# Kernel tuning notes

Hardware: AMD Instinct MI355X
Metric: run time of the kernel (lower is better)

Reference implementation:

```python
import jax, jax.numpy as jnp
import numpy as np
from jax import lax


def run_gru(seq, w_ih, w_hh, b_ih, b_hh):
    """PyTorch-convention GRU. seq: (T, N, E) -> outputs (T, N, H), h0 = 0."""
    H = w_hh.shape[1]
    gx = jnp.einsum('tne,ge->tng', seq, w_ih) + b_ih  # (T, N, 3H), precomputed input gates

    def step(h, gx_t):
        gh = h @ w_hh.T + b_hh
        xr, xz, xn = jnp.split(gx_t, 3, axis=-1)
        hr, hz, hn = jnp.split(gh, 3, axis=-1)
        r = jax.nn.sigmoid(xr + hr)
        z = jax.nn.sigmoid(xz + hz)
        n = jnp.tanh(xn + r * hn)
        h_new = (1.0 - z) * n + z * h
        return h_new, h_new

    h0 = jnp.zeros((seq.shape[1], H), dtype=seq.dtype)
    _, hs = lax.scan(step, h0, gx)
    return hs


def setup_inputs() -> dict:
    key = jax.random.key(0)
    ks = jax.random.split(key, 20)
    B, T, I, E, Ha, Hb, O = 32, 64, 256, 256, 256, 256, 1
    s = 0.05
    return {
        'x': jax.random.normal(ks[0], (B, T, I), dtype=jnp.float32),
        'emb_w': jax.random.normal(ks[1], (E, I), dtype=jnp.float32) * s,
        'emb_b': jax.random.normal(ks[2], (E,), dtype=jnp.float32) * s,
        'a_wih': jax.random.normal(ks[3], (3 * Ha, E), dtype=jnp.float32) * s,
        'a_whh': jax.random.normal(ks[4], (3 * Ha, Ha), dtype=jnp.float32) * s,
        'a_bih': jax.random.normal(ks[5], (3 * Ha,), dtype=jnp.float32) * s,
        'a_bhh': jax.random.normal(ks[6], (3 * Ha,), dtype=jnp.float32) * s,
        'b_wih': jax.random.normal(ks[7], (3 * Hb, E), dtype=jnp.float32) * s,
        'b_whh': jax.random.normal(ks[8], (3 * Hb, Hb), dtype=jnp.float32) * s,
        'b_bih': jax.random.normal(ks[9], (3 * Hb,), dtype=jnp.float32) * s,
        'b_bhh': jax.random.normal(ks[10], (3 * Hb,), dtype=jnp.float32) * s,
        'alpha_w': jax.random.normal(ks[11], (1, Ha), dtype=jnp.float32) * s,
        'alpha_b': jax.random.normal(ks[12], (1,), dtype=jnp.float32) * s,
        'beta_w': jax.random.normal(ks[13], (E, Hb), dtype=jnp.float32) * s,
        'beta_b': jax.random.normal(ks[14], (E,), dtype=jnp.float32) * s,
        'out_w': jax.random.normal(ks[15], (O, E), dtype=jnp.float32) * s,
        'out_b': jax.random.normal(ks[16], (O,), dtype=jnp.float32) * s,
    }


def reference(x, emb_w, emb_b, a_wih, a_whh, a_bih, a_bhh,
              b_wih, b_whh, b_bih, b_bhh, alpha_w, alpha_b,
              beta_w, beta_b, out_w, out_b):
    B, T, I = x.shape
    P = T - 1  # prefix lengths 1..T-1
    xt = jnp.transpose(x, (1, 0, 2))               # (T, B, I) time-major
    emb = jnp.einsum('tbi,ei->tbe', xt, emb_w) + emb_b  # (T, B, E)
    E = emb.shape[-1]

    # Reversed prefix p (length t=p+1): rev[p, k] = emb[p - k] for k < t, else 0.
    idx = jnp.arange(P)[:, None] - jnp.arange(T)[None, :]   # (P, T)
    valid = idx >= 0
    idxc = jnp.clip(idx, 0)
    rev = jnp.where(valid[:, :, None, None], emb[idxc], 0.0)  # (P, T, B, E)

    seq = jnp.transpose(rev, (1, 0, 2, 3)).reshape(T, P * B, E)  # (T, P*B, E)
    ha = run_gru(seq, a_wih, a_whh, a_bih, a_bhh)  # (T, P*B, Ha)
    hb = run_gru(seq, b_wih, b_whh, b_bih, b_bhh)  # (T, P*B, Hb)
    ha = jnp.transpose(ha.reshape(T, P, B, -1), (1, 0, 2, 3))  # (P, T, B, Ha)
    hb = jnp.transpose(hb.reshape(T, P, B, -1), (1, 0, 2, 3))

    # flip back within each prefix (same index map), then * 0.5 as in the source
    rows = jnp.arange(P)[:, None]
    fa = ha[rows, idxc] * 0.5   # (P, T, B, Ha); positions >= t are junk, masked below
    fb = hb[rows, idxc] * 0.5

    pre = jnp.einsum('ptbh,h->ptb', fa, alpha_w[0]) + alpha_b[0]
    logits = jnp.where(valid[:, :, None], pre, -jnp.inf)
    alpha = jax.nn.softmax(logits, axis=1)                       # softmax over time per prefix
    beta = jnp.tanh(jnp.einsum('ptbh,eh->ptbe', fb, beta_w) + beta_b)  # (P, T, B, E)

    # context: c_t = sum_j alpha * beta * emb[:t]  (alpha is 0 outside prefix)
    c = jnp.einsum('ptb,ptbe,tbe->pbe', alpha, beta, emb)        # (P, B, E)
    pred = (c @ out_w.T + out_b)                                  # (P, B, 1)
    pred = jnp.transpose(pred, (1, 0, 2))                         # (B, P, 1)

    # contribution weights; w_emb / w_out enter via .data in torch (no grad)
    w_emb = lax.stop_gradient(emb_w)
    w_out0 = lax.stop_gradient(out_w)[0]
    e = jnp.einsum('ptbe,e,ei->ptbi', beta, w_out0, w_emb)        # (P, T, B, I)
    denom = jnp.arange(1, P + 1, dtype=x.dtype)[:, None, None]    # mean over t visits
    g = jnp.einsum('ptb,ptbi,tbi->pbi', alpha, e, xt) / denom     # (P, B, I)
    weight = jnp.transpose(g, (1, 0, 2))                          # (B, P, I)
    return pred, weight
```

## Files before the change

kernel.cpp:

```cpp
#include <hip/hip_runtime.h>
#include <math.h>

#define B_   32
#define T_   64
#define P_   63
#define E_   256

typedef _Float16 half8 __attribute__((ext_vector_type(8)));
typedef _Float16 half4 __attribute__((ext_vector_type(4)));
typedef float    f32x4 __attribute__((ext_vector_type(4)));

__device__ __forceinline__ float sigmoidf_(float x) { return 1.0f / (1.0f + __expf(-x)); }
__device__ __forceinline__ float tanhfast_(float x) { float e = __expf(2.0f*x); return 1.0f - 2.0f/(e + 1.0f); }

__device__ __forceinline__ void barrier_lds_() {
    asm volatile("" ::: "memory");
    asm volatile("s_waitcnt lgkmcnt(0)" ::: "memory");
    __builtin_amdgcn_s_barrier();
    asm volatile("" ::: "memory");
}

__global__ __launch_bounds__(64) void k_prep(
    const float* __restrict__ awhh, const float* __restrict__ bwhh,
    const float* __restrict__ awih, const float* __restrict__ bwih,
    const float* __restrict__ beta_w, const float* __restrict__ emb_w, const float* __restrict__ out_w,
    _Float16* __restrict__ wfa, _Float16* __restrict__ wfb,
    _Float16* __restrict__ wifa, _Float16* __restrict__ wifb,
    _Float16* __restrict__ bwf, _Float16* __restrict__ mf)
{
    int bid = blockIdx.x, l = threadIdx.x;
    if (bid < 1664) {
        const float* W; _Float16* dst; float scale = 1.0f; int r;
        if (bid < 384)       { W = awhh;   dst = wfa;  r = bid; }
        else if (bid < 768)  { W = bwhh;   dst = wfb;  r = bid - 384; }
        else if (bid < 1152) { W = awih;   dst = wifa; r = bid - 768; }
        else if (bid < 1536) { W = bwih;   dst = wifb; r = bid - 1152; }
        else                 { W = beta_w; dst = bwf;  r = bid - 1536; scale = 0.5f; }
        int ot = r >> 3, kc = r & 7;
        int orow = ot * 16 + (l & 15);
        int c0   = kc * 32 + (l >> 4) * 8;
        half8 v;
        #pragma unroll
        for (int j = 0; j < 8; ++j) v[j] = (_Float16)(scale * W[(size_t)orow * 256 + c0 + j]);
        *reinterpret_cast<half8*>(&dst[((size_t)r * 64 + l) * 8]) = v;
    } else {
        int r = bid - 1664;
        int ot = r >> 3, kc = r & 7;
        int i  = ot * 16 + (l & 15);
        int e0 = kc * 32 + (l >> 4) * 8;
        half8 v;
        #pragma unroll
        for (int j = 0; j < 8; ++j) v[j] = (_Float16)(out_w[e0 + j] * emb_w[(size_t)(e0 + j) * 256 + i]);
        *reinterpret_cast<half8*>(&mf[((size_t)r * 64 + l) * 8]) = v;
    }
}

__global__ __launch_bounds__(256) void k_emb(const float* __restrict__ x,
                                             const float* __restrict__ emb_w,
                                             const float* __restrict__ emb_b,
                                             const float* __restrict__ out_w,
                                             _Float16* __restrict__ embh,
                                             _Float16* __restrict__ ewh,
                                             _Float16* __restrict__ xh) {
    int r0 = blockIdx.x * 8;
    int tid = threadIdx.x;
    __shared__ float xs[8][E_];
    for (int rr = 0; rr < 8; ++rr) {
        int row = r0 + rr, t = row >> 5, b = row & 31;
        float xv = x[((size_t)b * T_ + t) * E_ + tid];
        xs[rr][tid] = xv;
        xh[((size_t)b * T_ + t) * E_ + tid] = (_Float16)xv;
    }
    __syncthreads();
    float acc[8];
    #pragma unroll
    for (int rr = 0; rr < 8; ++rr) acc[rr] = 0.f;
    const float* wr = emb_w + (size_t)tid * E_;
    for (int c = 0; c < 256; c += 4) {
        float4 wv = *reinterpret_cast<const float4*>(wr + c);
        #pragma unroll
        for (int rr = 0; rr < 8; ++rr) {
            float4 ev = *reinterpret_cast<const float4*>(&xs[rr][c]);
            acc[rr] += wv.x * ev.x + wv.y * ev.y + wv.z * ev.z + wv.w * ev.w;
        }
    }
    float eb = emb_b[tid], ow = out_w[tid];
    #pragma unroll
    for (int rr = 0; rr < 8; ++rr) {
        float v = acc[rr] + eb;
        embh[(size_t)(r0 + rr) * E_ + tid] = (_Float16)v;
        ewh[(size_t)(r0 + rr) * E_ + tid]  = (_Float16)(v * ow);
    }
}

__global__ __launch_bounds__(512, 2) void k_gates2(
    const _Float16* __restrict__ embh,
    const _Float16* __restrict__ wifa, const _Float16* __restrict__ wifb,
    const float* __restrict__ abih, const float* __restrict__ abhh,
    const float* __restrict__ bbih, const float* __restrict__ bbhh,
    _Float16* __restrict__ gpa, _Float16* __restrict__ gpb)
{
    __shared__ _Float16 esw[32 * E_];
    int bid = blockIdx.x;
    int g = bid >> 6, t = bid & 63;
    const _Float16* wif = g ? wifb : wifa;
    const float* bih = g ? bbih : abih;
    const float* bhh = g ? bbhh : abhh;
    _Float16* gp = g ? gpb : gpa;
    int tid = threadIdx.x, w = tid >> 6, l = tid & 63, lg = l >> 4, lr = l & 15;

    #pragma unroll
    for (int q = 0; q < 2; ++q) {
        int idx = q * 512 + tid;
        int b = idx >> 5, e0 = (idx & 31) * 8;
        half8 v = *reinterpret_cast<const half8*>(&embh[((size_t)t * 32 + b) * E_ + e0]);
        *reinterpret_cast<half8*>(&esw[b * E_ + (e0 ^ ((b & 7) << 3))]) = v;
    }
    half8 aw[3][2][8];
    #pragma unroll
    for (int g3 = 0; g3 < 3; ++g3)
        #pragma unroll
        for (int i = 0; i < 2; ++i)
            #pragma unroll
            for (int kc = 0; kc < 8; ++kc)
                aw[g3][i][kc] = *reinterpret_cast<const half8*>(
                    &wif[(((size_t)(g3 * 16 + 2 * w + i) * 8 + kc) * 64 + l) * 8]);
    f32x4 acc[3][2][2];
    #pragma unroll
    for (int g3 = 0; g3 < 3; ++g3)
        #pragma unroll
        for (int i = 0; i < 2; ++i)
            #pragma unroll
            for (int rt = 0; rt < 2; ++rt)
                #pragma unroll
                for (int j = 0; j < 4; ++j) {
                    int d = g3 * 256 + 32 * w + 16 * i + lg * 4 + j;
                    acc[g3][i][rt][j] = bih[d] + ((g3 < 2) ? bhh[d] : 0.f);
                }
    __syncthreads();
    #pragma unroll
    for (int kc = 0; kc < 8; ++kc) {
        half8 eb[2];
        #pragma unroll
        for (int rt = 0; rt < 2; ++rt)
            eb[rt] = *reinterpret_cast<const half8*>(
                &esw[(rt * 16 + lr) * E_ + ((kc * 32 + lg * 8) ^ ((lr & 7) << 3))]);
        #pragma unroll
        for (int g3 = 0; g3 < 3; ++g3)
            #pragma unroll
            for (int i = 0; i < 2; ++i)
                #pragma unroll
                for (int rt = 0; rt < 2; ++rt)
                    acc[g3][i][rt] = __builtin_amdgcn_mfma_f32_16x16x32_f16(
                        aw[g3][i][kc], eb[rt], acc[g3][i][rt], 0, 0, 0);
    }
    #pragma unroll
    for (int g3 = 0; g3 < 3; ++g3)
        #pragma unroll
        for (int rt = 0; rt < 2; ++rt) {
            half8 v;
            #pragma unroll
            for (int i = 0; i < 2; ++i)
                #pragma unroll
                for (int j = 0; j < 4; ++j) v[i * 4 + j] = (_Float16)acc[g3][i][rt][j];
            *reinterpret_cast<half8*>(
                &gp[((((size_t)t * 2 + rt) * 8 + w) * 3 + g3) * 512 + l * 8]) = v;
        }
}

__global__ __launch_bounds__(512, 2) void k_gru_f(
    const _Float16* __restrict__ gpa, const _Float16* __restrict__ gpb,
    const _Float16* __restrict__ wfa, const _Float16* __restrict__ wfb,
    const float* __restrict__ abhh, const float* __restrict__ bbhh,
    const float* __restrict__ alpha_w, const float* __restrict__ alpha_b,
    float* __restrict__ pre, _Float16* __restrict__ hstore)
{
    extern __shared__ char smem[];
    half8*    wlds = reinterpret_cast<half8*>(smem);
    _Float16* hsp  = reinterpret_cast<_Float16*>(smem + 98304);
    float*    red  = reinterpret_cast<float*>(smem + 98304 + 16384);

    int bid = blockIdx.x;
    int p   = 62 - (bid >> 2);
    int g   = (bid >> 1) & 1;
    int bh  = bid & 1;
    int tid = threadIdx.x;
    int w = tid >> 6, l = tid & 63, lg = l >> 4, lr = l & 15;
    const _Float16* gp  = g ? gpb : gpa;
    const _Float16* wf  = g ? wfb : wfa;
    const float*    bhh = g ? bbhh : abhh;

    half8 wreg[3][2][6];
    #pragma unroll
    for (int g3 = 0; g3 < 3; ++g3)
        #pragma unroll
        for (int i = 0; i < 2; ++i) {
            int ot = g3 * 16 + 2 * w + i;
            #pragma unroll
            for (int kc = 0; kc < 6; ++kc)
                wreg[g3][i][kc] = *reinterpret_cast<const half8*>(&wf[((size_t)(ot * 8 + kc) * 64 + l) * 8]);
        }
    #pragma unroll
    for (int q = 0; q < 12; ++q) {
        int idx = q * 512 + tid;
        int ot = idx >> 7, kcs = (idx >> 6) & 1, l2 = idx & 63;
        wlds[idx] = *reinterpret_cast<const half8*>(&wf[((size_t)(ot * 8 + 6 + kcs) * 64 + l2) * 8]);
    }
    float bhn[2][4], awv[2][4];
    #pragma unroll
    for (int i = 0; i < 2; ++i)
        #pragma unroll
        for (int j = 0; j < 4; ++j) {
            int d = 32 * w + 16 * i + lg * 4 + j;
            bhn[i][j] = bhh[512 + d];
            awv[i][j] = alpha_w[d];
        }
    float ab = alpha_b[0];
    float hreg[2][4];
    #pragma unroll
    for (int i = 0; i < 2; ++i)
        #pragma unroll
        for (int j = 0; j < 4; ++j) hreg[i][j] = 0.f;
    __syncthreads();

    size_t tri = (size_t)p * (p + 1) / 2;

    for (int k = 0; k <= p; ++k) {
        int t_in = p - k;
        int wr = k & 1, rb = wr ^ 1;
        if (k > 0 && g == 0 && tid < 16) {
            float s = 0.f;
            #pragma unroll
            for (int q = 0; q < 8; ++q) s += red[(rb * 16 + tid) * 8 + q];
            pre[((size_t)p * T_ + (t_in + 1)) * B_ + bh * 16 + tid] = 0.5f * s + ab;
        }
        half8 gch[3];
        {
            const _Float16* gq = gp + (((size_t)(t_in * 2 + bh) * 8 + w) * 3) * 512 + l * 8;
            #pragma unroll
            for (int c = 0; c < 3; ++c)
                gch[c] = *reinterpret_cast<const half8*>(gq + (size_t)c * 512);
        }
        f32x4 acc[3][2];
        #pragma unroll
        for (int g3 = 0; g3 < 3; ++g3)
            #pragma unroll
            for (int i = 0; i < 2; ++i)
                #pragma unroll
                for (int j = 0; j < 4; ++j) acc[g3][i][j] = 0.f;
        if (k > 0) {
            half8 bhv[2];
            {
                int cb = (lg * 8) ^ ((lr & 7) << 3);
                bhv[0] = *reinterpret_cast<const half8*>(&hsp[(rb * 16 + lr) * 256 + cb]);
            }
            #pragma unroll
            for (int kc = 0; kc < 8; ++kc) {
                if (kc < 7) {
                    int cb = ((kc + 1) * 32 + lg * 8) ^ ((lr & 7) << 3);
                    bhv[(kc + 1) & 1] = *reinterpret_cast<const half8*>(&hsp[(rb * 16 + lr) * 256 + cb]);
                }
                if (kc < 6) {
                    #pragma unroll
                    for (int g3 = 0; g3 < 3; ++g3)
                        #pragma unroll
                        for (int i = 0; i < 2; ++i)
                            acc[g3][i] = __builtin_amdgcn_mfma_f32_16x16x32_f16(
                                wreg[g3][i][kc], bhv[kc & 1], acc[g3][i], 0, 0, 0);
                } else {
                    #pragma unroll
                    for (int g3 = 0; g3 < 3; ++g3)
                        #pragma unroll
                        for (int i = 0; i < 2; ++i) {
                            half8 wlv = wlds[((g3 * 16 + 2 * w + i) * 2 + (kc - 6)) * 64 + l];
                            acc[g3][i] = __builtin_amdgcn_mfma_f32_16x16x32_f16(
                                wlv, bhv[kc & 1], acc[g3][i], 0, 0, 0);
                        }
                }
            }
        }
        _Float16* hdst = hstore + ((tri + (size_t)k) * B_ + bh * 16 + lr) * (size_t)E_ + 32 * w + lg * 4;
        #pragma unroll
        for (int i = 0; i < 2; ++i) {
            half4 hh;
            #pragma unroll
            for (int j = 0; j < 4; ++j) {
                int e = i * 4 + j;
                float rg = sigmoidf_(acc[0][i][j] + (float)gch[0][e]);
                float zg = sigmoidf_(acc[1][i][j] + (float)gch[1][e]);
                float ng = tanhfast_((float)gch[2][e] + rg * (acc[2][i][j] + bhn[i][j]));
                float h  = (1.f - zg) * ng + zg * hreg[i][j];
                hreg[i][j] = h;
                hh[j] = (_Float16)h;
            }
            int ce = (32 * w + 16 * i + lg * 4) ^ ((lr & 7) << 3);
            *reinterpret_cast<half4*>(&hsp[(wr * 16 + lr) * 256 + ce]) = hh;
            if (g) *reinterpret_cast<half4*>(hdst + 16 * i) = hh;
        }
        if (!g) {
            float pa = 0.f;
            #pragma unroll
            for (int i = 0; i < 2; ++i)
                #pragma unroll
                for (int j = 0; j < 4; ++j) pa += hreg[i][j] * awv[i][j];
            pa += __shfl_xor(pa, 16, 64);
            pa += __shfl_xor(pa, 32, 64);
            if (l < 16) red[(wr * 16 + l) * 8 + w] = pa;
        }
        barrier_lds_();
    }
    if (g == 0 && tid < 16) {
        int wl = p & 1;
        float s = 0.f;
        #pragma unroll
        for (int q = 0; q < 8; ++q) s += red[(wl * 16 + tid) * 8 + q];
        pre[((size_t)p * T_ + 0) * B_ + bh * 16 + tid] = 0.5f * s + ab;
    }
}

__global__ __launch_bounds__(256, 1) void k_att(
    const _Float16* __restrict__ hH,
    const _Float16* __restrict__ bwf, const _Float16* __restrict__ mf,
    const float* __restrict__ beta_b,
    const float* __restrict__ pre,
    const _Float16* __restrict__ ewh, const _Float16* __restrict__ xh,
    const float* __restrict__ out_b,
    float* __restrict__ out)
{
    extern __shared__ char smem[];
    _Float16* hs   = reinterpret_cast<_Float16*>(smem);
    _Float16* es   = reinterpret_cast<_Float16*>(smem + 32768);
    _Float16* xs   = reinterpret_cast<_Float16*>(smem + 65536);
    float*    alds = reinterpret_cast<float*>(smem + 98304);
    float*    red  = reinterpret_cast<float*>(smem + 98304 + 256);
    int tid = threadIdx.x, w = tid >> 6, l = tid & 63, lg = l >> 4, lr = l & 15;

    half8 aw[4][8], am[4][8];
    #pragma unroll
    for (int ot = 0; ot < 4; ++ot)
        #pragma unroll
        for (int kc = 0; kc < 8; ++kc) {
            size_t fo = (((size_t)(4 * w + ot) * 8 + kc) * 64 + l) * 8;
            aw[ot][kc] = *reinterpret_cast<const half8*>(&bwf[fo]);
            am[ot][kc] = *reinterpret_cast<const half8*>(&mf[fo]);
        }
    float bb[4][4];
    #pragma unroll
    for (int ot = 0; ot < 4; ++ot)
        #pragma unroll
        for (int j = 0; j < 4; ++j)
            bb[ot][j] = beta_b[(4 * w + ot) * 16 + lg * 4 + j];
    float ob = out_b[0];

    for (int it = 0; it < 8; ++it) {
        int pair = blockIdx.x * 8 + it;
        int p = pair >> 5, b = pair & 31;
        size_t tri = (size_t)p * (p + 1) / 2;
        {
            int kr = tid >> 5, l32 = tid & 31, e0 = l32 * 8;
            #pragma unroll
            for (int q = 0; q < 8; ++q) {
                int k = q * 8 + kr;
                int sw = e0 ^ ((k & 7) << 3);
                half8 hv, ev;
                if (k <= p) {
                    hv = *reinterpret_cast<const half8*>(&hH[((tri + (size_t)(p - k)) * B_ + b) * 256 + e0]);
                    ev = *reinterpret_cast<const half8*>(&ewh[((size_t)k * B_ + b) * 256 + e0]);
                } else {
                    #pragma unroll
                    for (int j = 0; j < 8; ++j) { hv[j] = (_Float16)0.f; ev[j] = (_Float16)0.f; }
                }
                *reinterpret_cast<half8*>(&hs[k * 256 + sw]) = hv;
                *reinterpret_cast<half8*>(&es[k * 256 + sw]) = ev;
                *reinterpret_cast<half8*>(&xs[k * 256 + sw]) =
                    *reinterpret_cast<const half8*>(&xh[((size_t)b * T_ + k) * 256 + e0]);
            }
        }
        if (tid < 64) {
            float v = (tid <= p) ? pre[((size_t)p * T_ + tid) * B_ + b] : -3.4e38f;
            float m = v;
            #pragma unroll
            for (int off = 32; off > 0; off >>= 1) m = fmaxf(m, __shfl_xor(m, off, 64));
            float e = (tid <= p) ? __expf(v - m) : 0.f;
            float s = e;
            #pragma unroll
            for (int off = 32; off > 0; off >>= 1) s += __shfl_xor(s, off, 64);
            alds[tid] = e / s;
        }
        __syncthreads();
        f32x4 acc[4][4];
        #pragma unroll
        for (int ot = 0; ot < 4; ++ot)
            #pragma unroll
            for (int rt = 0; rt < 4; ++rt)
                #pragma unroll
                for (int j = 0; j < 4; ++j) acc[ot][rt][j] = bb[ot][j];
        #pragma unroll
        for (int kc = 0; kc < 8; ++kc) {
            half8 hb[4];
            #pragma unroll
            for (int rt = 0; rt < 4; ++rt)
                hb[rt] = *reinterpret_cast<const half8*>(&hs[(rt * 16 + lr) * 256 + ((kc * 32 + lg * 8) ^ ((lr & 7) << 3))]);
            #pragma unroll
            for (int ot = 0; ot < 4; ++ot)
                #pragma unroll
                for (int rt = 0; rt < 4; ++rt)
                    acc[ot][rt] = __builtin_amdgcn_mfma_f32_16x16x32_f16(aw[ot][kc], hb[rt], acc[ot][rt], 0, 0, 0);
        }
        float pv = 0.f;
        half4 ureg[4][4];
        #pragma unroll
        for (int ot = 0; ot < 4; ++ot)
            #pragma unroll
            for (int rt = 0; rt < 4; ++rt) {
                int k = rt * 16 + lr;
                float al = alds[k];
                int d0 = (4 * w + ot) * 16 + lg * 4;
                half4 ev4 = *reinterpret_cast<const half4*>(&es[k * 256 + (d0 ^ ((lr & 7) << 3))]);
                #pragma unroll
                for (int j = 0; j < 4; ++j) {
                    float u = al * tanhfast_(acc[ot][rt][j]);
                    ureg[ot][rt][j] = (_Float16)u;
                    pv += u * (float)ev4[j];
                }
            }
        __syncthreads();
        #pragma unroll
        for (int ot = 0; ot < 4; ++ot)
            #pragma unroll
            for (int rt = 0; rt < 4; ++rt) {
                int k = rt * 16 + lr;
                int d0 = (4 * w + ot) * 16 + lg * 4;
                *reinterpret_cast<half4*>(&hs[k * 256 + (d0 ^ ((lr & 7) << 3))]) = ureg[ot][rt];
            }
        #pragma unroll
        for (int off = 1; off < 64; off <<= 1) pv += __shfl_xor(pv, off, 64);
        if (l == 0) red[w] = pv;
        __syncthreads();
        if (tid == 0) out[(size_t)b * P_ + p] = red[0] + red[1] + red[2] + red[3] + ob;
        f32x4 a2[4][4];
        #pragma unroll
        for (int ot = 0; ot < 4; ++ot)
            #pragma unroll
            for (int rt = 0; rt < 4; ++rt)
                #pragma unroll
                for (int j = 0; j < 4; ++j) a2[ot][rt][j] = 0.f;
        #pragma unroll
        for (int kc = 0; kc < 8; ++kc) {
            half8 ub[4];
            #pragma unroll
            for (int rt = 0; rt < 4; ++rt)
                ub[rt] = *reinterpret_cast<const half8*>(&hs[(rt * 16 + lr) * 256 + ((kc * 32 + lg * 8) ^ ((lr & 7) << 3))]);
            #pragma unroll
            for (int ot = 0; ot < 4; ++ot)
                #pragma unroll
                for (int rt = 0; rt < 4; ++rt)
                    a2[ot][rt] = __builtin_amdgcn_mfma_f32_16x16x32_f16(am[ot][kc], ub[rt], a2[ot][rt], 0, 0, 0);
        }
        float r4[4][4];
        #pragma unroll
        for (int ot = 0; ot < 4; ++ot)
            #pragma unroll
            for (int j = 0; j < 4; ++j) r4[ot][j] = 0.f;
        #pragma unroll
        for (int ot = 0; ot < 4; ++ot)
            #pragma unroll
            for (int rt = 0; rt < 4; ++rt) {
                int k = rt * 16 + lr;
                int i0 = (4 * w + ot) * 16 + lg * 4;
                half4 xv4 = *reinterpret_cast<const half4*>(&xs[k * 256 + (i0 ^ ((lr & 7) << 3))]);
                #pragma unroll
                for (int j = 0; j < 4; ++j) r4[ot][j] += a2[ot][rt][j] * (float)xv4[j];
            }
        #pragma unroll
        for (int off = 1; off < 16; off <<= 1)
            #pragma unroll
            for (int ot = 0; ot < 4; ++ot)
                #pragma unroll
                for (int j = 0; j < 4; ++j) r4[ot][j] += __shfl_xor(r4[ot][j], off, 64);
        if (lr == 0) {
            float inv = 1.f / (float)(p + 1);
            #pragma unroll
            for (int ot = 0; ot < 4; ++ot) {
                f32x4 v;
                #pragma unroll
                for (int j = 0; j < 4; ++j) v[j] = r4[ot][j] * inv;
                *reinterpret_cast<f32x4*>(&out[2016 + ((size_t)b * P_ + p) * 256 + (4 * w + ot) * 16 + lg * 4]) = v;
            }
        }
        __syncthreads();
    }
}

extern "C" void kernel_launch(void* const* d_in, const int* in_sizes, int n_in,
                              void* d_out, int out_size, void* d_ws, size_t ws_size,
                              hipStream_t stream) {
    const float* x       = (const float*)d_in[0];
    const float* emb_w   = (const float*)d_in[1];
    const float* emb_b   = (const float*)d_in[2];
    const float* a_wih   = (const float*)d_in[3];
    const float* a_whh   = (const float*)d_in[4];
    const float* a_bih   = (const float*)d_in[5];
    const float* a_bhh   = (const float*)d_in[6];
    const float* b_wih   = (const float*)d_in[7];
    const float* b_whh   = (const float*)d_in[8];
    const float* b_bih   = (const float*)d_in[9];
    const float* b_bhh   = (const float*)d_in[10];
    const float* alpha_w = (const float*)d_in[11];
    const float* alpha_b = (const float*)d_in[12];
    const float* beta_w  = (const float*)d_in[13];
    const float* beta_b  = (const float*)d_in[14];
    const float* out_w   = (const float*)d_in[15];
    const float* out_b   = (const float*)d_in[16];
    float* out = (float*)d_out;

    float* ws = (float*)d_ws;
    _Float16* embh = (_Float16*)ws;
    _Float16* ewh  = embh + 524288;
    _Float16* xh   = ewh  + 524288;
    _Float16* gpa  = xh   + 524288;
    _Float16* gpb  = gpa  + 1572864;
    float* pre     = (float*)(gpb + 1572864);
    _Float16* wfa  = (_Float16*)(pre + 129024);
    _Float16* wfb  = wfa + 196608;
    _Float16* wifa = wfb + 196608;
    _Float16* wifb = wifa + 196608;
    _Float16* bwf  = wifb + 196608;
    _Float16* mf   = bwf + 65536;
    _Float16* hH   = mf  + 65536;

    const int GRU_LDS = 98304 + 16384 + 1024;
    (void)hipFuncSetAttribute((const void*)k_gru_f,
                              hipFuncAttributeMaxDynamicSharedMemorySize, GRU_LDS);
    const int ATT_LDS = 98304 + 256 + 64;
    (void)hipFuncSetAttribute((const void*)k_att,
                              hipFuncAttributeMaxDynamicSharedMemorySize, ATT_LDS);

    k_prep<<<1792, 64, 0, stream>>>(a_whh, b_whh, a_wih, b_wih, beta_w, emb_w, out_w,
                                    wfa, wfb, wifa, wifb, bwf, mf);
    k_emb<<<256, 256, 0, stream>>>(x, emb_w, emb_b, out_w, embh, ewh, xh);
    k_gates2<<<128, 512, 0, stream>>>(embh, wifa, wifb, a_bih, a_bhh, b_bih, b_bhh, gpa, gpb);
    k_gru_f<<<252, 512, GRU_LDS, stream>>>(gpa, gpb, wfa, wfb, a_bhh, b_bhh,
                                           alpha_w, alpha_b, pre, hH);
    k_att<<<252, 256, ATT_LDS, stream>>>(hH, bwf, mf, beta_b, pre, ewh, xh, out_b, out);
}
```

Baseline: 325.6 us.

## Fuse attention epilogue into GRU kernel using inter-block completion flags

Removes the separate attention kernel and runs its work at the tail of each GRU block. Each block publishes a release flag when its prefix finishes, then spins on the matching flags for the complementary prefix (62-p) so work is balanced across blocks processing long and short prefixes. This removes one kernel launch and the idle tail between kernels, at the cost of spin-waiting that relies on all 252 blocks being co-resident. The GRU update is also rewritten as ng + z*(h-ng) to save an operation.

```diff
diff --git a/kernel.cpp b/kernel.cpp
--- a/kernel.cpp
+++ b/kernel.cpp
@@ -173,7 +173,12 @@
     const _Float16* __restrict__ wfa, const _Float16* __restrict__ wfb,
     const float* __restrict__ abhh, const float* __restrict__ bbhh,
     const float* __restrict__ alpha_w, const float* __restrict__ alpha_b,
-    float* __restrict__ pre, _Float16* __restrict__ hstore)
+    const _Float16* __restrict__ bwf, const _Float16* __restrict__ mf,
+    const float* __restrict__ beta_b,
+    const _Float16* __restrict__ ewh, const _Float16* __restrict__ xh,
+    const float* __restrict__ out_b,
+    float* __restrict__ pre, _Float16* __restrict__ hstore,
+    int* __restrict__ flags, float* __restrict__ out)
 {
     extern __shared__ char smem[];
     half8*    wlds = reinterpret_cast<half8*>(smem);
@@ -289,7 +294,7 @@
                 float rg = sigmoidf_(acc[0][i][j] + (float)gch[0][e]);
                 float zg = sigmoidf_(acc[1][i][j] + (float)gch[1][e]);
                 float ng = tanhfast_((float)gch[2][e] + rg * (acc[2][i][j] + bhn[i][j]));
-                float h  = (1.f - zg) * ng + zg * hreg[i][j];
+                float h  = ng + zg * (hreg[i][j] - ng);
                 hreg[i][j] = h;
                 hh[j] = (_Float16)h;
             }
@@ -316,179 +321,183 @@
         for (int q = 0; q < 8; ++q) s += red[(wl * 16 + tid) * 8 + q];
         pre[((size_t)p * T_ + 0) * B_ + bh * 16 + tid] = 0.5f * s + ab;
     }
-}
-
-__global__ __launch_bounds__(256, 1) void k_att(
-    const _Float16* __restrict__ hH,
-    const _Float16* __restrict__ bwf, const _Float16* __restrict__ mf,
-    const float* __restrict__ beta_b,
-    const float* __restrict__ pre,
-    const _Float16* __restrict__ ewh, const _Float16* __restrict__ xh,
-    const float* __restrict__ out_b,
-    float* __restrict__ out)
-{
-    extern __shared__ char smem[];
-    _Float16* hs   = reinterpret_cast<_Float16*>(smem);
-    _Float16* es   = reinterpret_cast<_Float16*>(smem + 32768);
-    _Float16* xs   = reinterpret_cast<_Float16*>(smem + 65536);
-    float*    alds = reinterpret_cast<float*>(smem + 98304);
-    float*    red  = reinterpret_cast<float*>(smem + 98304 + 256);
-    int tid = threadIdx.x, w = tid >> 6, l = tid & 63, lg = l >> 4, lr = l & 15;
-
-    half8 aw[4][8], am[4][8];
-    #pragma unroll
-    for (int ot = 0; ot < 4; ++ot)
-        #pragma unroll
-        for (int kc = 0; kc < 8; ++kc) {
-            size_t fo = (((size_t)(4 * w + ot) * 8 + kc) * 64 + l) * 8;
-            aw[ot][kc] = *reinterpret_cast<const half8*>(&bwf[fo]);
-            am[ot][kc] = *reinterpret_cast<const half8*>(&mf[fo]);
-        }
-    float bb[4][4];
-    #pragma unroll
-    for (int ot = 0; ot < 4; ++ot)
-        #pragma unroll
-        for (int j = 0; j < 4; ++j)
-            bb[ot][j] = beta_b[(4 * w + ot) * 16 + lg * 4 + j];
-    float ob = out_b[0];
-
-    for (int it = 0; it < 8; ++it) {
-        int pair = blockIdx.x * 8 + it;
-        int p = pair >> 5, b = pair & 31;
-        size_t tri = (size_t)p * (p + 1) / 2;
-        {
-            int kr = tid >> 5, l32 = tid & 31, e0 = l32 * 8;
-            #pragma unroll
-            for (int q = 0; q < 8; ++q) {
-                int k = q * 8 + kr;
+
+    {
+        int pp = 62 - p;
+        size_t trip = (size_t)pp * (pp + 1) / 2;
+        half8 aw2[2][8], am2[2][8];
+        #pragma unroll
+        for (int i = 0; i < 2; ++i)
+            #pragma unroll
+            for (int kc = 0; kc < 8; ++kc) {
+                size_t fo = (((size_t)(2 * w + i) * 8 + kc) * 64 + l) * 8;
+                aw2[i][kc] = *reinterpret_cast<const half8*>(&bwf[fo]);
+                am2[i][kc] = *reinterpret_cast<const half8*>(&mf[fo]);
+            }
+        float bb2[2][4];
+        #pragma unroll
+        for (int i = 0; i < 2; ++i)
+            #pragma unroll
+            for (int j = 0; j < 4; ++j)
+                bb2[i][j] = beta_b[(2 * w + i) * 16 + lg * 4 + j];
+        float ob = out_b[0];
+        __threadfence();
+        __syncthreads();
+        if (tid == 0)
+            __hip_atomic_store(&flags[(g * 63 + p) * 2 + bh], 1,
+                               __ATOMIC_RELEASE, __HIP_MEMORY_SCOPE_AGENT);
+        #pragma unroll
+        for (int q = 0; q < 2; ++q) {
+            const int* fp_ = &flags[(q * 63 + pp) * 2 + bh];
+            while (__hip_atomic_load(fp_, __ATOMIC_ACQUIRE, __HIP_MEMORY_SCOPE_AGENT) == 0)
+                __builtin_amdgcn_s_sleep(8);
+        }
+        __syncthreads();
+        _Float16* hs   = reinterpret_cast<_Float16*>(smem);
+        _Float16* es2  = reinterpret_cast<_Float16*>(smem + 32768);
+        _Float16* xs2  = reinterpret_cast<_Float16*>(smem + 65536);
+        float*    alds = reinterpret_cast<float*>(smem + 98304);
+        float*    red2 = reinterpret_cast<float*>(smem + 98304 + 256);
+
+        for (int it = 0; it < 8; ++it) {
+            int b = bh * 16 + g * 8 + it;
+            #pragma unroll
+            for (int q = 0; q < 4; ++q) {
+                int idx = q * 512 + tid;
+                int k = idx >> 5, e0 = (idx & 31) * 8;
                 int sw = e0 ^ ((k & 7) << 3);
                 half8 hv, ev;
-                if (k <= p) {
-                    hv = *reinterpret_cast<const half8*>(&hH[((tri + (size_t)(p - k)) * B_ + b) * 256 + e0]);
+                if (k <= pp) {
+                    hv = *reinterpret_cast<const half8*>(&hstore[((trip + (size_t)(pp - k)) * B_ + b) * 256 + e0]);
                     ev = *reinterpret_cast<const half8*>(&ewh[((size_t)k * B_ + b) * 256 + e0]);
                 } else {
                     #pragma unroll
                     for (int j = 0; j < 8; ++j) { hv[j] = (_Float16)0.f; ev[j] = (_Float16)0.f; }
                 }
-                *reinterpret_cast<half8*>(&hs[k * 256 + sw]) = hv;
-                *reinterpret_cast<half8*>(&es[k * 256 + sw]) = ev;
-                *reinterpret_cast<half8*>(&xs[k * 256 + sw]) =
+                *reinterpret_cast<half8*>(&hs[k * 256 + sw])  = hv;
+                *reinterpret_cast<half8*>(&es2[k * 256 + sw]) = ev;
+                *reinterpret_cast<half8*>(&xs2[k * 256 + sw]) =
                     *reinterpret_cast<const half8*>(&xh[((size_t)b * T_ + k) * 256 + e0]);
             }
-        }
-        if (tid < 64) {
-            float v = (tid <= p) ? pre[((size_t)p * T_ + tid) * B_ + b] : -3.4e38f;
-            float m = v;
-            #pragma unroll
-            for (int off = 32; off > 0; off >>= 1) m = fmaxf(m, __shfl_xor(m, off, 64));
-            float e = (tid <= p) ? __expf(v - m) : 0.f;
-            float s = e;
-            #pragma unroll
-            for (int off = 32; off > 0; off >>= 1) s += __shfl_xor(s, off, 64);
-            alds[tid] = e / s;
-        }
-        __syncthreads();
-        f32x4 acc[4][4];
-        #pragma unroll
-        for (int ot = 0; ot < 4; ++ot)
-            #pragma unroll
-            for (int rt = 0; rt < 4; ++rt)
-                #pragma unroll
-                for (int j = 0; j < 4; ++j) acc[ot][rt][j] = bb[ot][j];
-        #pragma unroll
-        for (int kc = 0; kc < 8; ++kc) {
-            half8 hb[4];
-            #pragma unroll
-            for (int rt = 0; rt < 4; ++rt)
-                hb[rt] = *reinterpret_cast<const half8*>(&hs[(rt * 16 + lr) * 256 + ((kc * 32 + lg * 8) ^ ((lr & 7) << 3))]);
-            #pragma unroll
-            for (int ot = 0; ot < 4; ++ot)
+            if (tid < 64) {
+                float v = (tid <= pp) ? pre[((size_t)pp * T_ + tid) * B_ + b] : -3.4e38f;
+                float m = v;
+                #pragma unroll
+                for (int off = 32; off > 0; off >>= 1) m = fmaxf(m, __shfl_xor(m, off, 64));
+                float e = (tid <= pp) ? __expf(v - m) : 0.f;
+                float s = e;
+                #pragma unroll
+                for (int off = 32; off > 0; off >>= 1) s += __shfl_xor(s, off, 64);
+                alds[tid] = e / s;
+            }
+            __syncthreads();
+            f32x4 acc2[2][4];
+            #pragma unroll
+            for (int i = 0; i < 2; ++i)
                 #pragma unroll
                 for (int rt = 0; rt < 4; ++rt)
-                    acc[ot][rt] = __builtin_amdgcn_mfma_f32_16x16x32_f16(aw[ot][kc], hb[rt], acc[ot][rt], 0, 0, 0);
-        }
-        float pv = 0.f;
-        half4 ureg[4][4];
-        #pragma unroll
-        for (int ot = 0; ot < 4; ++ot)
-            #pragma unroll
-            for (int rt = 0; rt < 4; ++rt) {
-                int k = rt * 16 + lr;
-                float al = alds[k];
-                int d0 = (4 * w + ot) * 16 + lg * 4;
-                half4 ev4 = *reinterpret_cast<const half4*>(&es[k * 256 + (d0 ^ ((lr & 7) << 3))]);
-                #pragma unroll
-                for (int j = 0; j < 4; ++j) {
-                    float u = al * tanhfast_(acc[ot][rt][j]);
-                    ureg[ot][rt][j] = (_Float16)u;
-                    pv += u * (float)ev4[j];
-                }
-            }
-        __syncthreads();
-        #pragma unroll
-        for (int ot = 0; ot < 4; ++ot)
-            #pragma unroll
-            for (int rt = 0; rt < 4; ++rt) {
-                int k = rt * 16 + lr;
-                int d0 = (4 * w + ot) * 16 + lg * 4;
-                *reinterpret_cast<half4*>(&hs[k * 256 + (d0 ^ ((lr & 7) << 3))]) = ureg[ot][rt];
-            }
-        #pragma unroll
-        for (int off = 1; off < 64; off <<= 1) pv += __shfl_xor(pv, off, 64);
-        if (l == 0) red[w] = pv;
-        __syncthreads();
-        if (tid == 0) out[(size_t)b * P_ + p] = red[0] + red[1] + red[2] + red[3] + ob;
-        f32x4 a2[4][4];
-        #pragma unroll
-        for (int ot = 0; ot < 4; ++ot)
-            #pragma unroll
-            for (int rt = 0; rt < 4; ++rt)
-                #pragma unroll
-                for (int j = 0; j < 4; ++j) a2[ot][rt][j] = 0.f;
-        #pragma unroll
-        for (int kc = 0; kc < 8; ++kc) {
-            half8 ub[4];
-            #pragma unroll
-            for (int rt = 0; rt < 4; ++rt)
-                ub[rt] = *reinterpret_cast<const half8*>(&hs[(rt * 16 + lr) * 256 + ((kc * 32 + lg * 8) ^ ((lr & 7) << 3))]);
-            #pragma unroll
-            for (int ot = 0; ot < 4; ++ot)
+                    #pragma unroll
+                    for (int j = 0; j < 4; ++j) acc2[i][rt][j] = bb2[i][j];
+            #pragma unroll
+            for (int kc = 0; kc < 8; ++kc) {
+                half8 hb[4];
                 #pragma unroll
                 for (int rt = 0; rt < 4; ++rt)
-                    a2[ot][rt] = __builtin_amdgcn_mfma_f32_16x16x32_f16(am[ot][kc], ub[rt], a2[ot][rt], 0, 0, 0);
-        }
-        float r4[4][4];
-        #pragma unroll
-        for (int ot = 0; ot < 4; ++ot)
-            #pragma unroll
-            for (int j = 0; j < 4; ++j) r4[ot][j] = 0.f;
-        #pragma unroll
-        for (int ot = 0; ot < 4; ++ot)
-            #pragma unroll
-            for (int rt = 0; rt < 4; ++rt) {
-                int k = rt * 16 + lr;
-                int i0 = (4 * w + ot) * 16 + lg * 4;
-                half4 xv4 = *reinterpret_cast<const half4*>(&xs[k * 256 + (i0 ^ ((lr & 7) << 3))]);
-                #pragma unroll
-                for (int j = 0; j < 4; ++j) r4[ot][j] += a2[ot][rt][j] * (float)xv4[j];
-            }
-        #pragma unroll
-        for (int off = 1; off < 16; off <<= 1)
-            #pragma unroll
-            for (int ot = 0; ot < 4; ++ot)
-                #pragma unroll
-                for (int j = 0; j < 4; ++j) r4[ot][j] += __shfl_xor(r4[ot][j], off, 64);
-        if (lr == 0) {
-            float inv = 1.f / (float)(p + 1);
-            #pragma unroll
-            for (int ot = 0; ot < 4; ++ot) {
-                f32x4 v;
-                #pragma unroll
-                for (int j = 0; j < 4; ++j) v[j] = r4[ot][j] * inv;
-                *reinterpret_cast<f32x4*>(&out[2016 + ((size_t)b * P_ + p) * 256 + (4 * w + ot) * 16 + lg * 4]) = v;
-            }
-        }
-        __syncthreads();
+                    hb[rt] = *reinterpret_cast<const half8*>(&hs[(rt * 16 + lr) * 256 + ((kc * 32 + lg * 8) ^ ((lr & 7) << 3))]);
+                #pragma unroll
+                for (int i = 0; i < 2; ++i)
+                    #pragma unroll
+                    for (int rt = 0; rt < 4; ++rt)
+                        acc2[i][rt] = __builtin_amdgcn_mfma_f32_16x16x32_f16(aw2[i][kc], hb[rt], acc2[i][rt], 0, 0, 0);
+            }
+            float pv = 0.f;
+            half4 ureg[2][4];
+            #pragma unroll
+            for (int i = 0; i < 2; ++i)
+                #pragma unroll
+                for (int rt = 0; rt < 4; ++rt) {
+                    int k = rt * 16 + lr;
+                    float al = alds[k];
+                    int d0 = (2 * w + i) * 16 + lg * 4;
+                    half4 ev4 = *reinterpret_cast<const half4*>(&es2[k * 256 + (d0 ^ ((lr & 7) << 3))]);
+                    #pragma unroll
+                    for (int j = 0; j < 4; ++j) {
+                        float u = al * tanhfast_(acc2[i][rt][j]);
+                        ureg[i][rt][j] = (_Float16)u;
+                        pv += u * (float)ev4[j];
+                    }
+                }
+            __syncthreads();
+            #pragma unroll
+            for (int i = 0; i < 2; ++i)
+                #pragma unroll
+                for (int rt = 0; rt < 4; ++rt) {
+                    int k = rt * 16 + lr;
+                    int d0 = (2 * w + i) * 16 + lg * 4;
+                    *reinterpret_cast<half4*>(&hs[k * 256 + (d0 ^ ((lr & 7) << 3))]) = ureg[i][rt];
+                }
+            #pragma unroll
+            for (int off = 1; off < 64; off <<= 1) pv += __shfl_xor(pv, off, 64);
+            if (l == 0) red2[w] = pv;
+            __syncthreads();
+            if (tid == 0) {
+                float s = 0.f;
+                #pragma unroll
+                for (int q = 0; q < 8; ++q) s += red2[q];
+                out[(size_t)b * P_ + pp] = s + ob;
+            }
+            f32x4 a2[2][4];
+            #pragma unroll
+            for (int i = 0; i < 2; ++i)
+                #pragma unroll
+                for (int rt = 0; rt < 4; ++rt)
+                    #pragma unroll
+                    for (int j = 0; j < 4; ++j) a2[i][rt][j] = 0.f;
+            #pragma unroll
+            for (int kc = 0; kc < 8; ++kc) {
+                half8 ub[4];
+                #pragma unroll
+                for (int rt = 0; rt < 4; ++rt)
+                    ub[rt] = *reinterpret_cast<const half8*>(&hs[(rt * 16 + lr) * 256 + ((kc * 32 + lg * 8) ^ ((lr & 7) << 3))]);
+                #pragma unroll
+                for (int i = 0; i < 2; ++i)
+                    #pragma unroll
+                    for (int rt = 0; rt < 4; ++rt)
+                        a2[i][rt] = __builtin_amdgcn_mfma_f32_16x16x32_f16(am2[i][kc], ub[rt], a2[i][rt], 0, 0, 0);
+            }
+            float r4[2][4];
+            #pragma unroll
+            for (int i = 0; i < 2; ++i)
+                #pragma unroll
+                for (int j = 0; j < 4; ++j) r4[i][j] = 0.f;
+            #pragma unroll
+            for (int i = 0; i < 2; ++i)
+                #pragma unroll
+                for (int rt = 0; rt < 4; ++rt) {
+                    int k = rt * 16 + lr;
+                    int i0 = (2 * w + i) * 16 + lg * 4;
+                    half4 xv4 = *reinterpret_cast<const half4*>(&xs2[k * 256 + (i0 ^ ((lr & 7) << 3))]);
+                    #pragma unroll
+                    for (int j = 0; j < 4; ++j) r4[i][j] += a2[i][rt][j] * (float)xv4[j];
+                }
+            #pragma unroll
+            for (int off = 1; off < 16; off <<= 1)
+                #pragma unroll
+                for (int i = 0; i < 2; ++i)
+                    #pragma unroll
+                    for (int j = 0; j < 4; ++j) r4[i][j] += __shfl_xor(r4[i][j], off, 64);
+            if (lr == 0) {
+                float inv = 1.f / (float)(pp + 1);
+                #pragma unroll
+                for (int i = 0; i < 2; ++i) {
+                    f32x4 v;
+                    #pragma unroll
+                    for (int j = 0; j < 4; ++j) v[j] = r4[i][j] * inv;
+                    *reinterpret_cast<f32x4*>(&out[2016 + ((size_t)b * P_ + pp) * 256 + (2 * w + i) * 16 + lg * 4]) = v;
+                }
+            }
+            __syncthreads();
+        }
     }
 }
 
@@ -515,7 +524,8 @@
     float* out = (float*)d_out;
 
     float* ws = (float*)d_ws;
-    _Float16* embh = (_Float16*)ws;
+    int*  flags    = (int*)ws;
+    _Float16* embh = (_Float16*)(ws + 256);
     _Float16* ewh  = embh + 524288;
     _Float16* xh   = ewh  + 524288;
     _Float16* gpa  = xh   + 524288;
@@ -532,15 +542,13 @@
     const int GRU_LDS = 98304 + 16384 + 1024;
     (void)hipFuncSetAttribute((const void*)k_gru_f,
                               hipFuncAttributeMaxDynamicSharedMemorySize, GRU_LDS);
-    const int ATT_LDS = 98304 + 256 + 64;
-    (void)hipFuncSetAttribute((const void*)k_att,
-                              hipFuncAttributeMaxDynamicSharedMemorySize, ATT_LDS);
-
+
+    (void)hipMemsetAsync(flags, 0, 256 * sizeof(int), stream);
     k_prep<<<1792, 64, 0, stream>>>(a_whh, b_whh, a_wih, b_wih, beta_w, emb_w, out_w,
                                     wfa, wfb, wifa, wifb, bwf, mf);
     k_emb<<<256, 256, 0, stream>>>(x, emb_w, emb_b, out_w, embh, ewh, xh);
     k_gates2<<<128, 512, 0, stream>>>(embh, wifa, wifb, a_bih, a_bhh, b_bih, b_bhh, gpa, gpb);
     k_gru_f<<<252, 512, GRU_LDS, stream>>>(gpa, gpb, wfa, wfb, a_bhh, b_bhh,
-                                           alpha_w, alpha_b, pre, hH);
-    k_att<<<252, 256, ATT_LDS, stream>>>(hH, bwf, mf, beta_b, pre, ewh, xh, out_b, out);
+                                           alpha_w, alpha_b, bwf, mf, beta_b,
+                                           ewh, xh, out_b, pre, hH, flags, out);
 }
```

Result: slower. 463.6 us (+42.4%).

## Shrink attention kernel LDS and registers to run more blocks per CU

Applied to the files above, without the earlier changes.

The attention kernel no longer keeps the beta and contribution weight fragments in registers or stages the emb and x tiles in LDS. Weight fragments are loaded from global memory inside the MFMA loops, and the e and x vectors are read straight from global memory. LDS use falls from about 96KB to 32KB, launch bounds allow 3 blocks per CU, and the grid grows from 252 to 1008 blocks with 2 (p,b) pairs each instead of 8. The goal is higher occupancy and better latency hiding. The cost is repeated global/L2 weight traffic and uncoalesced epilogue loads, with padded rows beyond p masked in the prediction sum.

```diff
diff --git a/kernel.cpp b/kernel.cpp
--- a/kernel.cpp
+++ b/kernel.cpp
@@ -318,7 +318,7 @@
     }
 }
 
-__global__ __launch_bounds__(256, 1) void k_att(
+__global__ __launch_bounds__(256, 3) void k_att2(
     const _Float16* __restrict__ hH,
     const _Float16* __restrict__ bwf, const _Float16* __restrict__ mf,
     const float* __restrict__ beta_b,
@@ -329,21 +329,10 @@
 {
     extern __shared__ char smem[];
     _Float16* hs   = reinterpret_cast<_Float16*>(smem);
-    _Float16* es   = reinterpret_cast<_Float16*>(smem + 32768);
-    _Float16* xs   = reinterpret_cast<_Float16*>(smem + 65536);
-    float*    alds = reinterpret_cast<float*>(smem + 98304);
-    float*    red  = reinterpret_cast<float*>(smem + 98304 + 256);
+    float*    alds = reinterpret_cast<float*>(smem + 32768);
+    float*    red  = reinterpret_cast<float*>(smem + 32768 + 256);
     int tid = threadIdx.x, w = tid >> 6, l = tid & 63, lg = l >> 4, lr = l & 15;
 
-    half8 aw[4][8], am[4][8];
-    #pragma unroll
-    for (int ot = 0; ot < 4; ++ot)
-        #pragma unroll
-        for (int kc = 0; kc < 8; ++kc) {
-            size_t fo = (((size_t)(4 * w + ot) * 8 + kc) * 64 + l) * 8;
-            aw[ot][kc] = *reinterpret_cast<const half8*>(&bwf[fo]);
-            am[ot][kc] = *reinterpret_cast<const half8*>(&mf[fo]);
-        }
     float bb[4][4];
     #pragma unroll
     for (int ot = 0; ot < 4; ++ot)
@@ -352,8 +341,8 @@
             bb[ot][j] = beta_b[(4 * w + ot) * 16 + lg * 4 + j];
     float ob = out_b[0];
 
-    for (int it = 0; it < 8; ++it) {
-        int pair = blockIdx.x * 8 + it;
+    for (int it = 0; it < 2; ++it) {
+        int pair = blockIdx.x * 2 + it;
         int p = pair >> 5, b = pair & 31;
         size_t tri = (size_t)p * (p + 1) / 2;
         {
@@ -362,18 +351,14 @@
             for (int q = 0; q < 8; ++q) {
                 int k = q * 8 + kr;
                 int sw = e0 ^ ((k & 7) << 3);
-                half8 hv, ev;
+                half8 hv;
                 if (k <= p) {
                     hv = *reinterpret_cast<const half8*>(&hH[((tri + (size_t)(p - k)) * B_ + b) * 256 + e0]);
-                    ev = *reinterpret_cast<const half8*>(&ewh[((size_t)k * B_ + b) * 256 + e0]);
                 } else {
                     #pragma unroll
-                    for (int j = 0; j < 8; ++j) { hv[j] = (_Float16)0.f; ev[j] = (_Float16)0.f; }
+                    for (int j = 0; j < 8; ++j) hv[j] = (_Float16)0.f;
                 }
                 *reinterpret_cast<half8*>(&hs[k * 256 + sw]) = hv;
-                *reinterpret_cast<half8*>(&es[k * 256 + sw]) = ev;
-                *reinterpret_cast<half8*>(&xs[k * 256 + sw]) =
-                    *reinterpret_cast<const half8*>(&xh[((size_t)b * T_ + k) * 256 + e0]);
             }
         }
         if (tid < 64) {
@@ -402,10 +387,12 @@
             for (int rt = 0; rt < 4; ++rt)
                 hb[rt] = *reinterpret_cast<const half8*>(&hs[(rt * 16 + lr) * 256 + ((kc * 32 + lg * 8) ^ ((lr & 7) << 3))]);
             #pragma unroll
-            for (int ot = 0; ot < 4; ++ot)
+            for (int ot = 0; ot < 4; ++ot) {
+                half8 a = *reinterpret_cast<const half8*>(&bwf[(((size_t)(4 * w + ot) * 8 + kc) * 64 + l) * 8]);
                 #pragma unroll
                 for (int rt = 0; rt < 4; ++rt)
-                    acc[ot][rt] = __builtin_amdgcn_mfma_f32_16x16x32_f16(aw[ot][kc], hb[rt], acc[ot][rt], 0, 0, 0);
+                    acc[ot][rt] = __builtin_amdgcn_mfma_f32_16x16x32_f16(a, hb[rt], acc[ot][rt], 0, 0, 0);
+            }
         }
         float pv = 0.f;
         half4 ureg[4][4];
@@ -416,12 +403,12 @@
                 int k = rt * 16 + lr;
                 float al = alds[k];
                 int d0 = (4 * w + ot) * 16 + lg * 4;
-                half4 ev4 = *reinterpret_cast<const half4*>(&es[k * 256 + (d0 ^ ((lr & 7) << 3))]);
+                half4 ev4 = *reinterpret_cast<const half4*>(&ewh[((size_t)k * B_ + b) * 256 + d0]);
                 #pragma unroll
                 for (int j = 0; j < 4; ++j) {
                     float u = al * tanhfast_(acc[ot][rt][j]);
                     ureg[ot][rt][j] = (_Float16)u;
-                    pv += u * (float)ev4[j];
+                    pv += (k <= p) ? u * (float)ev4[j] : 0.f;
                 }
             }
         __syncthreads();
@@ -452,10 +439,12 @@
             for (int rt = 0; rt < 4; ++rt)
                 ub[rt] = *reinterpret_cast<const half8*>(&hs[(rt * 16 + lr) * 256 + ((kc * 32 + lg * 8) ^ ((lr & 7) << 3))]);
             #pragma unroll
-            for (int ot = 0; ot < 4; ++ot)
+            for (int ot = 0; ot < 4; ++ot) {
+                half8 a = *reinterpret_cast<const half8*>(&mf[(((size_t)(4 * w + ot) * 8 + kc) * 64 + l) * 8]);
                 #pragma unroll
                 for (int rt = 0; rt < 4; ++rt)
-                    a2[ot][rt] = __builtin_amdgcn_mfma_f32_16x16x32_f16(am[ot][kc], ub[rt], a2[ot][rt], 0, 0, 0);
+                    a2[ot][rt] = __builtin_amdgcn_mfma_f32_16x16x32_f16(a, ub[rt], a2[ot][rt], 0, 0, 0);
+            }
         }
         float r4[4][4];
         #pragma unroll
@@ -468,7 +457,7 @@
             for (int rt = 0; rt < 4; ++rt) {
                 int k = rt * 16 + lr;
                 int i0 = (4 * w + ot) * 16 + lg * 4;
-                half4 xv4 = *reinterpret_cast<const half4*>(&xs[k * 256 + (i0 ^ ((lr & 7) << 3))]);
+                half4 xv4 = *reinterpret_cast<const half4*>(&xh[((size_t)b * T_ + k) * 256 + i0]);
                 #pragma unroll
                 for (int j = 0; j < 4; ++j) r4[ot][j] += a2[ot][rt][j] * (float)xv4[j];
             }
@@ -532,8 +521,8 @@
     const int GRU_LDS = 98304 + 16384 + 1024;
     (void)hipFuncSetAttribute((const void*)k_gru_f,
                               hipFuncAttributeMaxDynamicSharedMemorySize, GRU_LDS);
-    const int ATT_LDS = 98304 + 256 + 64;
-    (void)hipFuncSetAttribute((const void*)k_att,
+    const int ATT_LDS = 32768 + 256 + 16;
+    (void)hipFuncSetAttribute((const void*)k_att2,
                               hipFuncAttributeMaxDynamicSharedMemorySize, ATT_LDS);
 
     k_prep<<<1792, 64, 0, stream>>>(a_whh, b_whh, a_wih, b_wih, beta_w, emb_w, out_w,
@@ -542,5 +531,5 @@
     k_gates2<<<128, 512, 0, stream>>>(embh, wifa, wifb, a_bih, a_bhh, b_bih, b_bhh, gpa, gpb);
     k_gru_f<<<252, 512, GRU_LDS, stream>>>(gpa, gpb, wfa, wfb, a_bhh, b_bhh,
                                            alpha_w, alpha_b, pre, hH);
-    k_att<<<252, 256, ATT_LDS, stream>>>(hH, bwf, mf, beta_b, pre, ewh, xh, out_b, out);
-}
+    k_att2<<<1008, 256, ATT_LDS, stream>>>(hH, bwf, mf, beta_b, pre, ewh, xh, out_b, out);
+}
```

New measurement: 477.9 us. 46.8% more time.
